# Optimization experiments

Hardware: AMD Instinct MI355X
Metric: run time of the kernel (lower is better)

## Reference

```python
import jax, jax.numpy as jnp
import numpy as np
import math

B, T, E, H = 8, 1024, 768, 12
D = E // H  # 64

def setup_inputs() -> dict:
    key = jax.random.key(0)
    ks = jax.random.split(key, 5)
    return {
        "x": jax.random.normal(ks[0], (B, T, E), dtype=jnp.float32),
        "w_attn": jax.random.normal(ks[1], (E, 3 * E), dtype=jnp.float32) * 0.02,
        "b_attn": jax.random.normal(ks[2], (3 * E,), dtype=jnp.float32) * 0.02,
        "w_proj": jax.random.normal(ks[3], (E, E), dtype=jnp.float32) * 0.02,
        "b_proj": jax.random.normal(ks[4], (E,), dtype=jnp.float32) * 0.02,
    }

def reference(x, w_attn, b_attn, w_proj, b_proj):
    b, t, e = x.shape
    h, d = H, E // H
    qkv = x @ w_attn + b_attn                      # [B,T,3E]
    q, k, v = jnp.split(qkv, 3, axis=2)
    q = q.reshape(b, t, h, d).transpose(0, 2, 1, 3)  # [B,H,T,D]
    k = k.reshape(b, t, h, d).transpose(0, 2, 1, 3)
    v = v.reshape(b, t, h, d).transpose(0, 2, 1, 3)
    scores = jnp.einsum('bhqd,bhkd->bhqk', q, k)     # [B,H,T,T]
    causal = jnp.tril(jnp.ones((t, t), dtype=bool))
    scores = jnp.where(causal[None, None], scores, -jnp.inf)
    attn = jax.nn.softmax(scores / jnp.float32(math.sqrt(d)), axis=-1)
    out = jnp.einsum('bhqk,bhkd->bhqd', attn, v)     # [B,H,T,D]
    out = out.transpose(0, 2, 1, 3).reshape(b, t, h * d)
    return out @ w_proj + b_proj
```

## Files before the change

kernel.cpp:

```cpp
#include <hip/hip_runtime.h>
#include <math.h>


#define B_ 8
#define T_ 1024
#define E_ 768
#define H_ 12
#define D_ 64
#define E3 (3 * E_)

typedef __attribute__((ext_vector_type(8))) short bf16x8;
typedef __attribute__((ext_vector_type(4))) float f32x4;

#define SCALE 0.18033688f

__device__ __forceinline__ unsigned short f2bf(float f) {
    unsigned int u = __builtin_bit_cast(unsigned int, f);
    u += 0x7fffu + ((u >> 16) & 1u);
    return (unsigned short)(u >> 16);
}

__device__ __forceinline__ void async_copy16(void* lds, const void* g) {
    __builtin_amdgcn_global_load_lds(
        (const __attribute__((address_space(1))) void*)g,
        (__attribute__((address_space(3))) void*)lds, 16, 0, 0);
}

#define NCVT 6144
#define NTA  (72 * 24)
#define NTP  (24 * 24)

__device__ __forceinline__ void transpose_tile(
    const float* __restrict__ W, unsigned short* __restrict__ Wt,
    int K, int N, int gx, int gy, unsigned short (*tile)[33])
{
    const int n0 = gx * 32, k0 = gy * 32;
    const int tx = threadIdx.x & 31, ty = threadIdx.x >> 5;
    #pragma unroll
    for (int i = 0; i < 4; ++i)
        tile[ty + i * 8][tx] = f2bf(W[(size_t)(k0 + ty + i * 8) * N + n0 + tx]);
    __syncthreads();
    #pragma unroll
    for (int i = 0; i < 4; ++i)
        Wt[(size_t)(n0 + ty + i * 8) * K + k0 + tx] = tile[tx][ty + i * 8];
}

__global__ __launch_bounds__(256) void prep_kernel(
    const float* __restrict__ x, unsigned short* __restrict__ x_bf,
    const float* __restrict__ w_attn, unsigned short* __restrict__ wat,
    const float* __restrict__ w_proj, unsigned short* __restrict__ wpt)
{
    __shared__ unsigned short tile[32][33];
    const int bid = blockIdx.x;
    if (bid < NCVT) {
        const int i = bid * 256 + threadIdx.x;
        float4 f = ((const float4*)x)[i];
        ushort4 o;
        o.x = f2bf(f.x); o.y = f2bf(f.y); o.z = f2bf(f.z); o.w = f2bf(f.w);
        ((ushort4*)x_bf)[i] = o;
    } else if (bid < NCVT + NTA) {
        const int t = bid - NCVT;
        transpose_tile(w_attn, wat, E_, E3, t % 72, t / 72, tile);
    } else {
        const int t = bid - NCVT - NTA;
        transpose_tile(w_proj, wpt, E_, E_, t % 24, t / 24, tile);
    }
}

template <typename OutT, int MODE, int BM, int BN, int WR, int WC>
__global__ __launch_bounds__(256) void gemm_mfma_kernel(
    const unsigned short* __restrict__ A,
    const unsigned short* __restrict__ Wt,
    const float* __restrict__ bias,
    OutT* __restrict__ C,
    unsigned short* __restrict__ vt,
    int M, int N, int K)
{
    constexpr int MT = BM / WR / 16;
    constexpr int NT = BN / WC / 16;
    constexpr int CA = BM / 32;
    constexpr int CB = BN / 32;
    constexpr int QBX = 768 / BN;
    constexpr int VBX = 1536 / BN;

    __shared__ unsigned short Abuf[BM * 64];
    __shared__ unsigned short Bbuf[BN * 64];

    const int tid = threadIdx.x;
    const int lane = tid & 63;
    const int w = tid >> 6;
    const int n16 = lane & 15;
    const int quad = lane >> 4;

    const int nbx = gridDim.x;
    const int lin = blockIdx.y * nbx + blockIdx.x;
    const int band_sz = 8 * nbx;
    const int band = lin / band_sz;
    const int rr = lin % band_sz;
    const int bm = (band * 8 + (rr & 7)) * BM;
    const int bx = rr >> 3;
    const int bn = bx * BN;

    const int wmbase = (w / WC) * (BM / WR);
    const int wnbase = (w % WC) * (BN / WC);

    const int lrow = lane >> 3;
    const int lcol = ((lane & 7) ^ lrow) * 8;

    f32x4 acc[MT][NT] = {};

    for (int k0 = 0; k0 < K; k0 += 64) {
        __syncthreads();
        #pragma unroll
        for (int i = 0; i < CA; ++i) {
            const int c = w * CA + i;
            const int row = c * 8 + lrow;
            async_copy16(&Abuf[c * 512], A + (size_t)(bm + row) * K + k0 + lcol);
        }
        #pragma unroll
        for (int i = 0; i < CB; ++i) {
            const int c = w * CB + i;
            const int row = c * 8 + lrow;
            async_copy16(&Bbuf[c * 512], Wt + (size_t)(bn + row) * K + k0 + lcol);
        }
        __syncthreads();

        #pragma unroll
        for (int kc = 0; kc < 2; ++kc) {
            bf16x8 af[MT], bf[NT];
            #pragma unroll
            for (int mt = 0; mt < MT; ++mt) {
                const int r = wmbase + mt * 16 + n16;
                af[mt] = *(const bf16x8*)&Abuf[r * 64 + ((kc * 4 + quad) ^ (r & 7)) * 8];
            }
            #pragma unroll
            for (int nt = 0; nt < NT; ++nt) {
                const int r = wnbase + nt * 16 + n16;
                bf[nt] = *(const bf16x8*)&Bbuf[r * 64 + ((kc * 4 + quad) ^ (r & 7)) * 8];
            }
            #pragma unroll
            for (int mt = 0; mt < MT; ++mt)
                #pragma unroll
                for (int nt = 0; nt < NT; ++nt)
                    acc[mt][nt] = __builtin_amdgcn_mfma_f32_16x16x32_bf16(
                        af[mt], bf[nt], acc[mt][nt], 0, 0, 0);
        }
    }

    if (MODE == 1 && bx >= VBX) {
        #pragma unroll
        for (int mt = 0; mt < MT; ++mt) {
            const int tt = bm + wmbase + mt * 16 + quad * 4;
            const size_t bb = (size_t)(tt >> 10) * 768;
            const int tin = tt & 1023;
            #pragma unroll
            for (int nt = 0; nt < NT; ++nt) {
                const int col = bn + wnbase + nt * 16 + n16;
                const int ch = col - 1536;
                const float bv = bias[col];
                ushort4 o4;
                o4.x = f2bf(acc[mt][nt][0] + bv);
                o4.y = f2bf(acc[mt][nt][1] + bv);
                o4.z = f2bf(acc[mt][nt][2] + bv);
                o4.w = f2bf(acc[mt][nt][3] + bv);
                *(ushort4*)&vt[(bb + ch) * 1024 + tin] = o4;
            }
        }
        return;
    }

    const bool scale_q = (MODE == 1) && (bx < QBX);
    #pragma unroll
    for (int mt = 0; mt < MT; ++mt) {
        #pragma unroll
        for (int r = 0; r < 4; ++r) {
            const size_t rowoff = (size_t)(bm + wmbase + mt * 16 + quad * 4 + r) * N;
            #pragma unroll
            for (int nt = 0; nt < NT; ++nt) {
                const int col = bn + wnbase + nt * 16 + n16;
                float v = acc[mt][nt][r] + bias[col];
                if (scale_q) v *= SCALE;
                if constexpr (sizeof(OutT) == 2) C[rowoff + col] = (OutT)f2bf(v);
                else                             C[rowoff + col] = (OutT)v;
            }
        }
    }
}

#define BKEY 128
#define VSTR 136

__global__ __launch_bounds__(256) void flash_attn_kernel(
    const unsigned short* __restrict__ qkv,
    const unsigned short* __restrict__ vt,
    unsigned short* __restrict__ out)
{
    __shared__ unsigned short Ks[BKEY * 64];
    __shared__ unsigned short Vts[64 * BKEY];
    __shared__ unsigned short Ps[4 * 16 * VSTR];

    const int tid = threadIdx.x;
    const int idx = blockIdx.x;
    const int head = idx % 96;
    const int p    = idx / 96;
    const int h = head % H_;
    const int b = head / H_;

    const int lane = tid & 63;
    const int w    = tid >> 6;
    const int n16  = lane & 15;
    const int quad = lane >> 4;

    const size_t base = (size_t)b * T_ * E3;
    const unsigned short* qbase = qkv + base + h * D_;
    const unsigned short* kbase = qkv + base + E_ + h * D_;
    const unsigned short* vtb   = vt + (size_t)(b * H_ + h) * 64 * 1024;

    const int lrow = lane >> 3;
    const int lcol = ((lane & 7) ^ lrow) * 8;
    const int vr4 = lane >> 4;
    const int vc  = lane & 15;

    unsigned short* pw = &Ps[w * 16 * VSTR];

    const int qtA = p, qtB = 15 - p;
    const int nIterA = (qtA + 2) >> 1;
    const int nIterB = (qtB + 2) >> 1;
    const int wqA = qtA * 64 + w * 16;
    const int wqB = qtB * 64 + w * 16;

    const unsigned short* qrpA = qbase + (size_t)(wqA + n16) * E3 + quad * 8;
    bf16x8 qfA0 = *(const bf16x8*)qrpA;
    bf16x8 qfA1 = *(const bf16x8*)(qrpA + 32);
    const unsigned short* qrpB = qbase + (size_t)(wqB + n16) * E3 + quad * 8;
    bf16x8 qfB0 = *(const bf16x8*)qrpB;
    bf16x8 qfB1 = *(const bf16x8*)(qrpB + 32);

    f32x4 oA[4] = {}, oB[4] = {};
    float lsA = 0.f, lsB = 0.f;

    for (int it = 0; it < nIterB; ++it) {
        const int k0 = it * BKEY;
        __syncthreads();

        #pragma unroll
        for (int i = 0; i < 4; ++i) {
            const int c = w * 4 + i;
            const int row = c * 8 + lrow;
            async_copy16(&Ks[c * 512], kbase + (size_t)(k0 + row) * E3 + lcol);
        }
        #pragma unroll
        for (int i = 0; i < 4; ++i) {
            const int j = w * 4 + i;
            const int row = 4 * j + vr4;
            async_copy16(&Vts[4 * j * BKEY],
                         vtb + (size_t)row * 1024 + k0 + ((vc ^ (row & 15)) * 8));
        }
        __syncthreads();

        auto phase = [&](bf16x8 qf0, bf16x8 qf1, f32x4* o, float& lsum,
                         int wave_q_min) {
            int knt_lim = ((wave_q_min + 15 - k0) >> 4) + 1;
            if (knt_lim > 8) knt_lim = 8;
            const int ks_lim = (knt_lim + 1) >> 1;
            int Ab2 = wave_q_min - k0 - 15;
            int kfull = Ab2 < 0 ? 0 : (Ab2 >> 4) + 1;
            if (kfull > 8) kfull = 8;

            const int qcol = wave_q_min + n16;

            f32x4 s[8];
            #pragma unroll
            for (int knt = 0; knt < 8; ++knt) {
                if (knt < knt_lim) {
                    const int r = knt * 16 + n16;
                    bf16x8 kf0 = *(const bf16x8*)&Ks[r * 64 + ((0 + quad) ^ (r & 7)) * 8];
                    bf16x8 kf1 = *(const bf16x8*)&Ks[r * 64 + ((4 + quad) ^ (r & 7)) * 8];
                    f32x4 acc = {0.f, 0.f, 0.f, 0.f};
                    acc = __builtin_amdgcn_mfma_f32_16x16x32_bf16(kf0, qf0, acc, 0, 0, 0);
                    acc = __builtin_amdgcn_mfma_f32_16x16x32_bf16(kf1, qf1, acc, 0, 0, 0);
                    s[knt] = acc;
                }
            }
            #pragma unroll
            for (int knt = 0; knt < 8; ++knt) {
                if (knt >= kfull) {
                    const int krow = k0 + knt * 16 + quad * 4;
                    #pragma unroll
                    for (int r = 0; r < 4; ++r) {
                        float v = (knt < knt_lim) ? s[knt][r] : -1e30f;
                        if (krow + r > qcol) v = -1e30f;
                        s[knt][r] = v;
                    }
                }
            }

            #pragma unroll
            for (int knt = 0; knt < 8; ++knt) {
                float pv0 = __builtin_amdgcn_exp2f(s[knt][0]);
                float pv1 = __builtin_amdgcn_exp2f(s[knt][1]);
                float pv2 = __builtin_amdgcn_exp2f(s[knt][2]);
                float pv3 = __builtin_amdgcn_exp2f(s[knt][3]);
                lsum += (pv0 + pv1) + (pv2 + pv3);
                unsigned int u0 = __builtin_bit_cast(unsigned int, pv0);
                unsigned int u1 = __builtin_bit_cast(unsigned int, pv1);
                unsigned int u2 = __builtin_bit_cast(unsigned int, pv2);
                unsigned int u3 = __builtin_bit_cast(unsigned int, pv3);
                uint2 pk;
                pk.x = ((u0 + 0x8000u) >> 16) | ((u1 + 0x8000u) & 0xffff0000u);
                pk.y = ((u2 + 0x8000u) >> 16) | ((u3 + 0x8000u) & 0xffff0000u);
                *(uint2*)&pw[n16 * VSTR + knt * 16 + quad * 4] = pk;
            }

            #pragma unroll
            for (int ks = 0; ks < 4; ++ks) {
                if (ks < ks_lim) {
                    bf16x8 pf = *(const bf16x8*)&pw[n16 * VSTR + ks * 32 + quad * 8];
                    #pragma unroll
                    for (int dt = 0; dt < 4; ++dt) {
                        const int row = dt * 16 + n16;
                        bf16x8 vf = *(const bf16x8*)&Vts[row * BKEY +
                                        (((ks * 4 + quad) ^ n16) * 8)];
                        o[dt] = __builtin_amdgcn_mfma_f32_16x16x32_bf16(pf, vf, o[dt], 0, 0, 0);
                    }
                }
            }
        };

        phase(qfB0, qfB1, oB, lsB, wqB);
        if (it < nIterA) phase(qfA0, qfA1, oA, lsA, wqA);
    }

    lsA += __shfl_xor(lsA, 16); lsA += __shfl_xor(lsA, 32);
    lsB += __shfl_xor(lsB, 16); lsB += __shfl_xor(lsB, 32);

    #pragma unroll
    for (int r = 0; r < 4; ++r) {
        const float invA = 1.f / __shfl(lsA, quad * 4 + r);
        unsigned short* orowA = out + ((size_t)b * T_ + wqA + quad * 4 + r) * E_ + h * D_;
        #pragma unroll
        for (int dt = 0; dt < 4; ++dt)
            orowA[dt * 16 + n16] = f2bf(oA[dt][r] * invA);
        const float invB = 1.f / __shfl(lsB, quad * 4 + r);
        unsigned short* orowB = out + ((size_t)b * T_ + wqB + quad * 4 + r) * E_ + h * D_;
        #pragma unroll
        for (int dt = 0; dt < 4; ++dt)
            orowB[dt * 16 + n16] = f2bf(oB[dt][r] * invB);
    }
}

extern "C" void kernel_launch(void* const* d_in, const int* in_sizes, int n_in,
                              void* d_out, int out_size, void* d_ws, size_t ws_size,
                              hipStream_t stream)
{
    const float* x      = (const float*)d_in[0];
    const float* w_attn = (const float*)d_in[1];
    const float* b_attn = (const float*)d_in[2];
    const float* w_proj = (const float*)d_in[3];
    const float* b_proj = (const float*)d_in[4];
    float* out = (float*)d_out;

    const int M = B_ * T_;

    unsigned short* x_bf   = (unsigned short*)d_ws;
    unsigned short* wat    = x_bf + (size_t)M * E_;
    unsigned short* wpt    = wat + (size_t)E3 * E_;
    unsigned short* qkv_bf = wpt + (size_t)E_ * E_;
    unsigned short* att_bf = qkv_bf + (size_t)M * E3;
    unsigned short* vt_bf  = att_bf + (size_t)M * E_;

    prep_kernel<<<NCVT + NTA + NTP, 256, 0, stream>>>(x, x_bf, w_attn, wat, w_proj, wpt);

    gemm_mfma_kernel<unsigned short, 1, 128, 128, 2, 2>
        <<<dim3(E3 / 128, M / 128), 256, 0, stream>>>(
        x_bf, wat, b_attn, qkv_bf, vt_bf, M, E3, E_);

    flash_attn_kernel<<<B_ * H_ * 8, 256, 0, stream>>>(qkv_bf, vt_bf, att_bf);

    gemm_mfma_kernel<float, 0, 64, 128, 2, 2>
        <<<dim3(E_ / 128, M / 64), 256, 0, stream>>>(
        att_bf, wpt, b_proj, out, nullptr, M, E_, E_);
}
```

Before: 198.9 us.

## Replace QKV GEMM with 256x256-tile 8-wave pipelined MFMA kernel

After: 200.4 us. Within noise of the previous version (+0.7%).

```diff
diff --git a/kernel.cpp b/kernel.cpp
--- a/kernel.cpp
+++ b/kernel.cpp
@@ -67,6 +67,181 @@
     }
 }
 
+
+__global__ __launch_bounds__(512, 2) void gemm_qkv_256(
+    const unsigned short* __restrict__ A,
+    const unsigned short* __restrict__ Wt,
+    const float* __restrict__ bias,
+    unsigned short* __restrict__ C,
+    unsigned short* __restrict__ vt)
+{
+    constexpr int K = 768;
+    constexpr int N = E3;
+    constexpr int NI = 6;
+
+    extern __shared__ unsigned short lds[];
+    unsigned short* const Ab0 = lds;
+    unsigned short* const Ab1 = lds + 16384;
+    unsigned short* const Bb0 = lds + 32768;
+    unsigned short* const Bb1 = lds + 49152;
+
+    const int tid  = threadIdx.x;
+    const int lane = tid & 63;
+    const int w    = tid >> 6;
+    const int wm   = w >> 2;
+    const int wn   = w & 3;
+    const int n16  = lane & 15;
+    const int quad = lane >> 4;
+    const int l7   = lane & 7;
+    const int lrow = lane >> 3;
+    const int lcol = (l7 ^ lrow) * 8;
+
+    const int lin  = blockIdx.x;
+    const int work = (lin & 7) * 36 + (lin >> 3);
+    const int by = work / 9, bx = work % 9;
+    const int bm = by * 256, bn = bx * 256;
+
+    const unsigned short* Asrc = A  + (size_t)(bm + w * 16 + lrow) * K + lcol;
+    const unsigned short* Bsrc = Wt + (size_t)(bn + w * 16 + lrow) * K + lcol;
+
+    auto stgA = [&](unsigned short* buf, int kt, int h) {
+        #pragma unroll
+        for (int i = 0; i < 2; ++i)
+            async_copy16(&buf[h * 8192 + (w * 2 + i) * 512],
+                         Asrc + (size_t)(h * 128 + i * 8) * K + kt * 64);
+    };
+    auto stgB = [&](unsigned short* buf, int kt, int h) {
+        #pragma unroll
+        for (int i = 0; i < 2; ++i)
+            async_copy16(&buf[h * 8192 + (w * 2 + i) * 512],
+                         Bsrc + (size_t)(h * 128 + i * 8) * K + kt * 64);
+    };
+
+    bf16x8 afr[8], b0f[4], b1f[4];
+    f32x4 acc[8][4] = {};
+
+#define LDA(buf, qm) { \
+    _Pragma("unroll") \
+    for (int ml = 0; ml < 4; ++ml) { \
+        const int r = wm * 16 + ((qm) * 4 + ml) * 32 + n16; \
+        const unsigned short* rp = (buf) + r * 64; \
+        afr[ml * 2 + 0] = *(const bf16x8*)&rp[((0 + quad) ^ l7) * 8]; \
+        afr[ml * 2 + 1] = *(const bf16x8*)&rp[((4 + quad) ^ l7) * 8]; \
+    } }
+#define LDB(bfr, buf, qn) { \
+    _Pragma("unroll") \
+    for (int nl = 0; nl < 2; ++nl) { \
+        const int r = wn * 16 + ((qn) * 2 + nl) * 64 + n16; \
+        const unsigned short* rp = (buf) + r * 64; \
+        bfr[nl * 2 + 0] = *(const bf16x8*)&rp[((0 + quad) ^ l7) * 8]; \
+        bfr[nl * 2 + 1] = *(const bf16x8*)&rp[((4 + quad) ^ l7) * 8]; \
+    } }
+#define MM(qm, qn, bfr) { \
+    _Pragma("unroll") \
+    for (int ml = 0; ml < 4; ++ml) \
+    _Pragma("unroll") \
+    for (int nl = 0; nl < 2; ++nl) \
+    _Pragma("unroll") \
+    for (int kk = 0; kk < 2; ++kk) \
+        acc[(qm) * 4 + ml][(qn) * 2 + nl] = __builtin_amdgcn_mfma_f32_16x16x32_bf16( \
+            afr[ml * 2 + kk], bfr[nl * 2 + kk], acc[(qm) * 4 + ml][(qn) * 2 + nl], 0, 0, 0); }
+
+#define BARR  __builtin_amdgcn_s_barrier()
+#define LGKM0 asm volatile("s_waitcnt lgkmcnt(0)" ::: "memory")
+#define VM6   asm volatile("s_waitcnt vmcnt(6)" ::: "memory")
+#define VM0   asm volatile("s_waitcnt vmcnt(0)" ::: "memory")
+#define PRI1  __builtin_amdgcn_s_setprio(1)
+#define PRI0  __builtin_amdgcn_s_setprio(0)
+
+    stgA(Ab0, 0, 0); stgB(Bb0, 0, 0); stgB(Bb0, 0, 1); stgA(Ab0, 0, 1);
+    stgA(Ab1, 1, 0); stgB(Bb1, 1, 0); stgB(Bb1, 1, 1);
+    VM6; BARR;
+
+    #pragma unroll 1
+    for (int I = 0; I < NI - 1; ++I) {
+        const int u = 2 * I;
+        LDA(Ab0, 0); LDB(b0f, Bb0, 0);
+        stgA(Ab1, u + 1, 1);
+        BARR; LGKM0; PRI1; MM(0, 0, b0f); PRI0; BARR;
+        LDB(b1f, Bb0, 1);
+        stgA(Ab0, u + 2, 0);
+        BARR; LGKM0; PRI1; MM(0, 1, b1f); PRI0; BARR;
+        LDA(Ab0, 1);
+        stgB(Bb0, u + 2, 0);
+        BARR; LGKM0; PRI1; MM(1, 1, b1f); PRI0; BARR;
+        stgB(Bb0, u + 2, 1);
+        BARR; LGKM0; PRI1; MM(1, 0, b0f); PRI0; VM6; BARR;
+        LDA(Ab1, 0); LDB(b0f, Bb1, 0);
+        stgA(Ab0, u + 2, 1);
+        BARR; LGKM0; PRI1; MM(0, 0, b0f); PRI0; BARR;
+        LDB(b1f, Bb1, 1);
+        stgA(Ab1, u + 3, 0);
+        BARR; LGKM0; PRI1; MM(0, 1, b1f); PRI0; BARR;
+        LDA(Ab1, 1);
+        stgB(Bb1, u + 3, 0);
+        BARR; LGKM0; PRI1; MM(1, 1, b1f); PRI0; BARR;
+        stgB(Bb1, u + 3, 1);
+        BARR; LGKM0; PRI1; MM(1, 0, b0f); PRI0; VM6; BARR;
+    }
+
+    LDA(Ab0, 0); LDB(b0f, Bb0, 0);
+    stgA(Ab1, 11, 1);
+    BARR; LGKM0; PRI1; MM(0, 0, b0f); PRI0; BARR;
+    LDB(b1f, Bb0, 1);
+    BARR; LGKM0; PRI1; MM(0, 1, b1f); PRI0; BARR;
+    LDA(Ab0, 1);
+    BARR; LGKM0; PRI1; MM(1, 1, b1f); PRI0; BARR;
+    BARR; PRI1; MM(1, 0, b0f); PRI0; VM0; BARR;
+    LDA(Ab1, 0); LDB(b0f, Bb1, 0);
+    BARR; LGKM0; PRI1; MM(0, 0, b0f); PRI0; BARR;
+    LDB(b1f, Bb1, 1);
+    BARR; LGKM0; PRI1; MM(0, 1, b1f); PRI0; BARR;
+    LDA(Ab1, 1);
+    BARR; LGKM0; PRI1; MM(1, 1, b1f); PRI0; BARR;
+    PRI1; MM(1, 0, b0f); PRI0;
+
+#undef LDA
+#undef LDB
+#undef MM
+
+    if (bx >= 6) {
+        #pragma unroll
+        for (int m = 0; m < 8; ++m) {
+            const int tt = bm + wm * 16 + m * 32 + quad * 4;
+            const size_t bb = (size_t)(tt >> 10) * 768;
+            const int tin = tt & 1023;
+            #pragma unroll
+            for (int n = 0; n < 4; ++n) {
+                const int col = bn + wn * 16 + n * 64 + n16;
+                const int ch = col - 1536;
+                const float bv = bias[col];
+                ushort4 o4;
+                o4.x = f2bf(acc[m][n][0] + bv);
+                o4.y = f2bf(acc[m][n][1] + bv);
+                o4.z = f2bf(acc[m][n][2] + bv);
+                o4.w = f2bf(acc[m][n][3] + bv);
+                *(ushort4*)&vt[(bb + ch) * 1024 + tin] = o4;
+            }
+        }
+    } else {
+        const bool scale_q = bx < 3;
+        #pragma unroll
+        for (int m = 0; m < 8; ++m) {
+            #pragma unroll
+            for (int r = 0; r < 4; ++r) {
+                const size_t rowoff = (size_t)(bm + wm * 16 + m * 32 + quad * 4 + r) * N;
+                #pragma unroll
+                for (int n = 0; n < 4; ++n) {
+                    const int col = bn + wn * 16 + n * 64 + n16;
+                    float v = acc[m][n][r] + bias[col];
+                    if (scale_q) v *= SCALE;
+                    C[rowoff + col] = f2bf(v);
+                }
+            }
+        }
+    }
+}
+
 template <typename OutT, int MODE, int BM, int BN, int WR, int WC>
 __global__ __launch_bounds__(256) void gemm_mfma_kernel(
     const unsigned short* __restrict__ A,
@@ -369,11 +544,17 @@
     unsigned short* att_bf = qkv_bf + (size_t)M * E3;
     unsigned short* vt_bf  = att_bf + (size_t)M * E_;
 
+    static bool qkv_attr_set = false;
+    if (!qkv_attr_set) {
+        hipFuncSetAttribute((const void*)gemm_qkv_256,
+                            hipFuncAttributeMaxDynamicSharedMemorySize, 131072);
+        qkv_attr_set = true;
+    }
+
     prep_kernel<<<NCVT + NTA + NTP, 256, 0, stream>>>(x, x_bf, w_attn, wat, w_proj, wpt);
 
-    gemm_mfma_kernel<unsigned short, 1, 128, 128, 2, 2>
-        <<<dim3(E3 / 128, M / 128), 256, 0, stream>>>(
-        x_bf, wat, b_attn, qkv_bf, vt_bf, M, E3, E_);
+    gemm_qkv_256<<<dim3(288), dim3(512), 131072, stream>>>(
+        x_bf, wat, b_attn, qkv_bf, vt_bf);
 
     flash_attn_kernel<<<B_ * H_ * 8, 256, 0, stream>>>(qkv_bf, vt_bf, att_bf);
 
```
